# Optimization experiments

Hardware: AMD Instinct MI355X
Metric: run time of the kernel (lower is better)

## Reference

```python
import jax, jax.numpy as jnp
import numpy as np

N_QUBITS = 10
INPUT_DIM = 49
ENC_LAMBDA = float(np.pi)
ENC_BETA_MAX = 1.0
BATCH = 2048
LOGIT_SCALE_MIN, LOGIT_SCALE_MAX = 0.5, 80.0
LOGIT_CLAMP = 30.0

# arch_mat rows: [control, target, op, axis, feature]; op: ENC=1, ROT=2, CNOT=3; 1-indexed, 0=none.
def _build_arch_mat():
    cols = []
    for b in range(3):
        for q in range(N_QUBITS):  # encoding RY gates
            cols.append((0, q + 1, 1, 2, (b * N_QUBITS + q) % INPUT_DIM + 1))
        for q in range(N_QUBITS):  # trainable RX gates
            cols.append((0, q + 1, 2, 1, 0))
        for q in range(N_QUBITS - 1):  # CNOT chain
            cols.append((q + 1, q + 2, 3, 0, 0))
    return np.asarray(cols, dtype=np.int64).T  # (5, L)

ARCH_MAT = _build_arch_mat()
N_THETA = int(((ARCH_MAT[2] == 2) & (ARCH_MAT[1] > 0) & (ARCH_MAT[3] > 0)).sum())


def _apply_rot(state, ax, q, theta):
    # state: (B, 2,...,2) complex64; theta: scalar or (B,)
    st = jnp.moveaxis(state, 1 + q, -1)
    half = 0.5 * theta
    c, s = jnp.cos(half), jnp.sin(half)
    if c.ndim == 1:  # per-sample angle -> broadcast over remaining qubit axes
        shape = (-1,) + (1,) * (st.ndim - 2)
        c, s = c.reshape(shape), s.reshape(shape)
    s0, s1 = st[..., 0], st[..., 1]
    if ax == 1:  # RX
        n0 = c * s0 - 1j * s * s1
        n1 = c * s1 - 1j * s * s0
    elif ax == 2:  # RY
        n0 = c * s0 - s * s1
        n1 = c * s1 + s * s0
    else:  # RZ
        n0 = (c - 1j * s) * s0
        n1 = (c + 1j * s) * s1
    return jnp.moveaxis(jnp.stack([n0, n1], axis=-1), -1, 1 + q)


def _apply_cnot(state, cq, tq):
    st = jnp.moveaxis(state, (1 + cq, 1 + tq), (-2, -1))
    st = jnp.stack([st[..., 0, :], st[..., 1, ::-1]], axis=-2)
    return jnp.moveaxis(st, (-2, -1), (1 + cq, 1 + tq))


def _circuit(x, theta, enc_alpha_raw, enc_beta_raw):
    B = x.shape[0]
    state = jnp.zeros((B,) + (2,) * N_QUBITS, jnp.complex64)
    state = state.at[(slice(None),) + (0,) * N_QUBITS].set(1.0)
    alpha = jax.nn.softplus(enc_alpha_raw) + 1e-6  # (D,)
    beta = jnp.tanh(enc_beta_raw) * ENC_BETA_MAX   # (D,)
    rot_idx = 0
    for l in range(ARCH_MAT.shape[1]):  # static structural loop over gates
        c, t, op, ax, f1 = (int(v) for v in ARCH_MAT[:, l])
        if op == 1 and t > 0 and ax > 0 and f1 > 0:
            fi = f1 - 1
            ang = ENC_LAMBDA * (alpha[fi] * x[:, fi] + beta[fi])  # (B,)
            state = _apply_rot(state, ax, t - 1, ang)
        elif op == 2 and t > 0 and ax > 0:
            state = _apply_rot(state, ax, t - 1, theta[rot_idx])
            rot_idx += 1
        elif op == 3 and c > 0 and t > 0 and c != t:
            state = _apply_cnot(state, c - 1, t - 1)
    probs = state.real ** 2 + state.imag ** 2  # (B, 2,...,2)
    exps = []
    for q in range(N_QUBITS):  # <Z_q> = p(q=0) - p(q=1)
        p = jnp.moveaxis(probs, 1 + q, -1).reshape(B, -1, 2).sum(axis=1)
        exps.append(p[:, 0] - p[:, 1])
    return jnp.stack(exps, axis=1)  # (B, n_qubits)


def setup_inputs() -> dict:
    key = jax.random.key(0)
    k = jax.random.split(key, 4)
    x = jax.random.normal(k[0], (BATCH, INPUT_DIM), jnp.float32)
    theta = jnp.clip(0.01 * jax.random.normal(k[1], (N_THETA,), jnp.float32), -0.1, 0.1)
    a0 = float(np.log(np.exp(1.0) - 1.0))  # softplus^-1(enc_alpha_init=1.0)
    enc_alpha_raw = jnp.full((INPUT_DIM,), a0, jnp.float32)
    enc_beta_raw = jnp.zeros((INPUT_DIM,), jnp.float32)  # arctanh(0)=0
    head_w = 0.02 * jax.random.normal(k[2], (1, N_QUBITS), jnp.float32)
    bound = 1.0 / float(np.sqrt(N_QUBITS))
    head_b = jax.random.uniform(k[3], (1,), jnp.float32, -bound, bound)
    logit_scale = jnp.asarray(1.0, jnp.float32)
    return {"x": x, "theta": theta, "enc_alpha_raw": enc_alpha_raw, "enc_beta_raw": enc_beta_raw,
            "head_w": head_w, "head_b": head_b, "logit_scale": logit_scale}


def reference(x, theta, enc_alpha_raw, enc_beta_raw, head_w, head_b, logit_scale):
    exps = _circuit(x, theta, enc_alpha_raw, enc_beta_raw)  # (B, n_qubits)
    raw = exps @ head_w.T + head_b                          # (B, 1)
    scale = jnp.clip(logit_scale, LOGIT_SCALE_MIN, LOGIT_SCALE_MAX)
    return jnp.clip(scale * raw, -LOGIT_CLAMP, LOGIT_CLAMP)
```

## Files before the change

### kernel.cpp

```cpp
#include <hip/hip_runtime.h>
#include <math.h>


#define PI_F 3.14159265358979323846f

typedef unsigned v2u __attribute__((ext_vector_type(2)));

#if defined(__has_builtin)
#if __has_builtin(__builtin_amdgcn_permlane16_swap)
#define HAVE_PL16 1
#endif
#if __has_builtin(__builtin_amdgcn_permlane32_swap)
#define HAVE_PL32 1
#endif
#endif

__device__ __forceinline__ float rdlane(float v, int l) {
    return __int_as_float(__builtin_amdgcn_readlane(__float_as_int(v), l));
}

__device__ __forceinline__ float xor1p(float v) {
    return __int_as_float(__builtin_amdgcn_update_dpp(
        0, __float_as_int(v), 0xB1, 0xF, 0xF, true));
}
__device__ __forceinline__ float xor2p(float v) {
    return __int_as_float(__builtin_amdgcn_update_dpp(
        0, __float_as_int(v), 0x4E, 0xF, 0xF, true));
}
__device__ __forceinline__ float xor4p(float v) {
    int t = __builtin_amdgcn_update_dpp(0, __float_as_int(v), 0x1B, 0xF, 0xF, true);
    t = __builtin_amdgcn_update_dpp(0, t, 0x141, 0xF, 0xF, true);
    return __int_as_float(t);
}
__device__ __forceinline__ float xor8p(float v) {
    return __int_as_float(__builtin_amdgcn_update_dpp(
        0, __float_as_int(v), 0x128, 0xF, 0xF, true));
}
__device__ __forceinline__ float xor16p(float v, bool hi) {
#ifdef HAVE_PL16
    v2u r = __builtin_amdgcn_permlane16_swap(
        (unsigned)__float_as_int(v), (unsigned)__float_as_int(v), false, false);
    return __int_as_float((int)(hi ? r.x : r.y));
#else
    return __shfl_xor(v, 16);
#endif
}
__device__ __forceinline__ float xor32p(float v, bool hi) {
#ifdef HAVE_PL32
    v2u r = __builtin_amdgcn_permlane32_swap(
        (unsigned)__float_as_int(v), (unsigned)__float_as_int(v), false, false);
    return __int_as_float((int)(hi ? r.x : r.y));
#else
    return __shfl_xor(v, 32);
#endif
}

template<int Q>
__device__ __forceinline__ float lane_xor(float v, bool hi) {
    if constexpr (Q == 0) return xor1p(v);
    else if constexpr (Q == 1) return xor2p(v);
    else if constexpr (Q == 2) return xor4p(v);
    else if constexpr (Q == 3) return xor8p(v);
    else if constexpr (Q == 4) return xor16p(v, hi);
    else return xor32p(v, hi);
}

template<bool NEG>
__device__ __forceinline__ float2 cgate(const float2 ar2, const float2 ai2,
                                        const float2 br2, const float2 bi2,
                                        const float2 v, const float2 w) {
    float2 acc;
    asm("v_pk_mul_f32 %0, %1, %2" : "=v"(acc) : "v"(ar2), "v"(v));
    if constexpr (!NEG) {
        asm("v_pk_fma_f32 %0, %1, %2, %0 op_sel:[0,1,0] op_sel_hi:[1,0,1] neg_lo:[0,1,0]"
            : "+v"(acc) : "v"(ai2), "v"(v));
        asm("v_pk_fma_f32 %0, %1, %2, %0" : "+v"(acc) : "v"(br2), "v"(w));
    } else {
        asm("v_pk_fma_f32 %0, %1, %2, %0 op_sel:[0,1,0] op_sel_hi:[1,0,1] neg_lo:[1,1,0] neg_hi:[1,0,0]"
            : "+v"(acc) : "v"(ai2), "v"(v));
        asm("v_pk_fma_f32 %0, %1, %2, %0 neg_lo:[1,0,0] neg_hi:[1,0,0]"
            : "+v"(acc) : "v"(br2), "v"(w));
    }
    asm("v_pk_fma_f32 %0, %1, %2, %0 op_sel:[0,1,0] op_sel_hi:[1,0,1] neg_lo:[0,1,0]"
        : "+v"(acc) : "v"(bi2), "v"(w));
    return acc;
}

template<int Q>
__device__ __forceinline__ void lane_gate(float2 (&st)[8], int lane,
                                          float ar, float ai, float br, float bi) {
    const bool hi = (lane & (1 << Q)) != 0;
    const float aiL = hi ? -ai : ai;
    const float brL = hi ? -br : br;
    const float2 ar2 = make_float2(ar, ar);
    const float2 ai2 = make_float2(aiL, aiL);
    const float2 br2 = make_float2(brL, brL);
    const float2 bi2 = make_float2(bi, bi);
    #pragma unroll
    for (int r = 0; r < 8; ++r) {
        float2 p;
        p.x = lane_xor<Q>(st[r].x, hi);
        p.y = lane_xor<Q>(st[r].y, hi);
        st[r] = cgate<false>(ar2, ai2, br2, bi2, st[r], p);
    }
}

template<int RB>
__device__ __forceinline__ void reg_gate(float2 (&st)[8],
                                         float ar, float ai, float br, float bi) {
    const float2 ar2 = make_float2(ar, ar);
    const float2 ai2 = make_float2(ai, ai);
    const float2 br2 = make_float2(br, br);
    const float2 bi2 = make_float2(bi, bi);
    #pragma unroll
    for (int r = 0; r < 8; ++r) {
        if ((r & RB) == 0) {
            const int r1 = r | RB;
            const float2 v0 = st[r], v1 = st[r1];
            st[r]  = cgate<false>(ar2, ai2, br2, bi2, v0, v1);
            st[r1] = cgate<true >(ar2, ai2, br2, bi2, v1, v0);
        }
    }
}

__global__ __launch_bounds__(256, 4) void cqv_kernel(
    const float* __restrict__ x,
    const float* __restrict__ theta,
    const float* __restrict__ alpha_raw,
    const float* __restrict__ beta_raw,
    const float* __restrict__ head_w,
    const float* __restrict__ head_b,
    const float* __restrict__ logit_scale,
    float* __restrict__ out,
    int batch)
{
    const int lane = threadIdx.x & 63;
    const int wavid = threadIdx.x >> 6;
    const int p  = wavid >> 1;
    const int wv = wavid & 1;
    const int s = blockIdx.x * 2 + p;
    if (s >= batch) return;

    __shared__ float2 lds[2][2][8][2][64];
    __shared__ float pbuf[2][2];

    const int l5 = (lane >> 5) & 1;
    const int srcLane = lane ^ ((lane & 31) << 1);

    const int g = (lane < 30) ? lane : 0;
    const float alpha = log1pf(__expf(alpha_raw[g])) + 1e-6f;
    const float beta  = tanhf(beta_raw[g]);
    const float halfE = 0.5f * PI_F * (alpha * x[s * 49 + g] + beta);
    float cE, sE, cT, sT;
    __sincosf(halfE, &sE, &cE);
    __sincosf(0.5f * theta[g], &sT, &cT);

    float2 st[8];

    {
        float u0r[10], u0i[10], u1r[10], u1i[10];
        #pragma unroll
        for (int q = 0; q < 10; ++q) {
            const float ce = rdlane(cE, q), se = rdlane(sE, q);
            const float ct = rdlane(cT, q), s_t = rdlane(sT, q);
            u0r[q] = ct * ce;  u0i[q] = -s_t * se;
            u1r[q] = ct * se;  u1i[q] = -s_t * ce;
        }
        float plr = 1.f, pli = 0.f;
        #pragma unroll
        for (int q = 0; q < 6; ++q) {
            const bool bq = (lane >> q) & 1;
            const float wr = bq ? u1r[q] : u0r[q];
            const float wi = bq ? u1i[q] : u0i[q];
            const float nr = plr * wr - pli * wi;
            const float ni = plr * wi + pli * wr;
            plr = nr; pli = ni;
        }
        const float w9r = wv ? u1r[9] : u0r[9], w9i = wv ? u1i[9] : u0i[9];
        float t67r[4], t67i[4], t89r[2], t89i[2];
        #pragma unroll
        for (int a = 0; a < 4; ++a) {
            const float w6r = (a & 1) ? u1r[6] : u0r[6], w6i = (a & 1) ? u1i[6] : u0i[6];
            const float w7r = (a & 2) ? u1r[7] : u0r[7], w7i = (a & 2) ? u1i[7] : u0i[7];
            t67r[a] = w6r * w7r - w6i * w7i;  t67i[a] = w6r * w7i + w6i * w7r;
        }
        #pragma unroll
        for (int k = 0; k < 2; ++k) {
            const float w8r = k ? u1r[8] : u0r[8], w8i = k ? u1i[8] : u0i[8];
            t89r[k] = w8r * w9r - w8i * w9i;  t89i[k] = w8r * w9i + w8i * w9r;
        }
        #pragma unroll
        for (int r = 0; r < 8; ++r) {
            const float ar = t67r[r & 3] * t89r[r >> 2] - t67i[r & 3] * t89i[r >> 2];
            const float ai = t67r[r & 3] * t89i[r >> 2] + t67i[r & 3] * t89r[r >> 2];
            st[r].x = ar * plr - ai * pli;
            st[r].y = ar * pli + ai * plr;
        }
    }

    {
        #pragma unroll
        for (int r = 0; r < 8; ++r) lds[0][p][r][wv][lane] = st[r];
        __syncthreads();
        #pragma unroll
        for (int r = 0; r < 8; ++r) {
            const int sReg = (r ^ ((r & 3) << 1)) ^ l5;
            const int k9 = wv ^ (r >> 2);
            st[r] = lds[0][p][sReg][k9][srcLane];
        }
    }

    #pragma unroll 1
    for (int b = 1; b < 3; ++b) {
        const int base = b * 10;
#define GATE_PARAMS(Q) \
        const float ce = rdlane(cE, base + (Q)), se = rdlane(sE, base + (Q)); \
        const float ct = rdlane(cT, base + (Q)), s_t = rdlane(sT, base + (Q));
#define APPLY_LANE_GATE(Q) { GATE_PARAMS(Q) \
        lane_gate<Q>(st, lane, ct * ce, -s_t * se, -ct * se, -s_t * ce); }
#define APPLY_REG_GATE(Q, RB) { GATE_PARAMS(Q) \
        reg_gate<RB>(st, ct * ce, -s_t * se, -ct * se, -s_t * ce); }
        APPLY_LANE_GATE(0)
        APPLY_LANE_GATE(1)
        APPLY_LANE_GATE(2)
        APPLY_LANE_GATE(3)
        APPLY_LANE_GATE(4)
        APPLY_LANE_GATE(5)
        APPLY_REG_GATE(6, 1)
        APPLY_REG_GATE(7, 2)
        APPLY_REG_GATE(8, 4)

        const int db = b & 1;
        GATE_PARAMS(9)
        const float ar = ct * ce, ai = -s_t * se, br = -ct * se, bi = -s_t * ce;
        const float2 ar2 = make_float2(ar, ar), ai2 = make_float2(ai, ai);
        const float2 br2 = make_float2(br, br), bi2 = make_float2(bi, bi);
        #pragma unroll
        for (int r = 0; r < 8; ++r) lds[db][p][r][wv][lane] = st[r];
        __syncthreads();
        #pragma unroll
        for (int r = 0; r < 8; ++r) {
            const int sReg = (r ^ ((r & 3) << 1)) ^ l5;
            const int k9 = wv ^ (r >> 2);
            const float2 v = lds[db][p][sReg][k9][srcLane];
            const float2 w = lds[db][p][sReg][k9 ^ 1][srcLane];
            if (k9 == 0) st[r] = cgate<false>(ar2, ai2, br2, bi2, v, w);
            else         st[r] = cgate<true >(ar2, ai2, br2, bi2, v, w);
        }
#undef GATE_PARAMS
#undef APPLY_LANE_GATE
#undef APPLY_REG_GATE
    }

    float w[10];
    #pragma unroll
    for (int q = 0; q < 10; ++q) w[q] = head_w[q];
    float wlane = wv ? -w[9] : w[9];
    #pragma unroll
    for (int q = 0; q < 6; ++q) wlane += ((lane >> q) & 1) ? -w[q] : w[q];
    float acc = 0.f, psum = 0.f;
    #pragma unroll
    for (int r = 0; r < 8; ++r) {
        const float pw = st[r].x * st[r].x + st[r].y * st[r].y;
        const float wr = ((r & 1) ? -w[6] : w[6]) + ((r & 2) ? -w[7] : w[7])
                       + ((r & 4) ? -w[8] : w[8]);
        psum += pw;
        acc = fmaf(wr, pw, acc);
    }
    float partial = fmaf(wlane, psum, acc);
    #pragma unroll
    for (int off = 32; off >= 1; off >>= 1) partial += __shfl_xor(partial, off);

    if (lane == 0) pbuf[p][wv] = partial;
    __syncthreads();
    if (lane == 0 && wv == 0) {
        const float scale = fminf(fmaxf(logit_scale[0], 0.5f), 80.f);
        const float raw = pbuf[p][0] + pbuf[p][1] + head_b[0];
        out[s] = fminf(fmaxf(scale * raw, -30.f), 30.f);
    }
}

extern "C" void kernel_launch(void* const* d_in, const int* in_sizes, int n_in,
                              void* d_out, int out_size, void* d_ws, size_t ws_size,
                              hipStream_t stream) {
    const int B = in_sizes[0] / 49;
    dim3 block(256);
    dim3 grid((B + 1) / 2);
    cqv_kernel<<<grid, block, 0, stream>>>(
        (const float*)d_in[0], (const float*)d_in[1], (const float*)d_in[2],
        (const float*)d_in[3], (const float*)d_in[4], (const float*)d_in[5],
        (const float*)d_in[6], (float*)d_out, B);
}
```

Baseline: 81.23 us.

## Use one sample per block and skip the final qubit-transpose via parity-aware readout

Launches one 128-thread block per sample instead of packing two samples into a 256-thread block, so each __syncthreads only spans two waves. The last layer's LDS exchange now reads only the partner wave's value at the same index rather than permuting lanes and registers. The Z-expectation readout is rewritten with prefix-parity signs so it works in the untransposed layout. This trims shuffle and address work in the final stage but doubles the block count and carries a risk of sign errors in the parity mapping.

```diff
diff --git a/kernel.cpp b/kernel.cpp
--- a/kernel.cpp
+++ b/kernel.cpp
@@ -123,7 +123,7 @@
     }
 }
 
-__global__ __launch_bounds__(256, 4) void cqv_kernel(
+__global__ __launch_bounds__(128, 4) void cqv_kernel(
     const float* __restrict__ x,
     const float* __restrict__ theta,
     const float* __restrict__ alpha_raw,
@@ -135,14 +135,11 @@
     int batch)
 {
     const int lane = threadIdx.x & 63;
-    const int wavid = threadIdx.x >> 6;
-    const int p  = wavid >> 1;
-    const int wv = wavid & 1;
-    const int s = blockIdx.x * 2 + p;
-    if (s >= batch) return;
-
-    __shared__ float2 lds[2][2][8][2][64];
-    __shared__ float pbuf[2][2];
+    const int wv = threadIdx.x >> 6;
+    const int s = blockIdx.x;
+
+    __shared__ float2 lds[2][8][2][64];
+    __shared__ float pbuf[2];
 
     const int l5 = (lane >> 5) & 1;
     const int srcLane = lane ^ ((lane & 31) << 1);
@@ -200,82 +197,101 @@
 
     {
         #pragma unroll
-        for (int r = 0; r < 8; ++r) lds[0][p][r][wv][lane] = st[r];
+        for (int r = 0; r < 8; ++r) lds[0][r][wv][lane] = st[r];
         __syncthreads();
         #pragma unroll
         for (int r = 0; r < 8; ++r) {
             const int sReg = (r ^ ((r & 3) << 1)) ^ l5;
             const int k9 = wv ^ (r >> 2);
-            st[r] = lds[0][p][sReg][k9][srcLane];
-        }
-    }
-
-    #pragma unroll 1
-    for (int b = 1; b < 3; ++b) {
-        const int base = b * 10;
-#define GATE_PARAMS(Q) \
-        const float ce = rdlane(cE, base + (Q)), se = rdlane(sE, base + (Q)); \
-        const float ct = rdlane(cT, base + (Q)), s_t = rdlane(sT, base + (Q));
-#define APPLY_LANE_GATE(Q) { GATE_PARAMS(Q) \
+            st[r] = lds[0][sReg][k9][srcLane];
+        }
+    }
+
+#define GATE_PARAMS(BASE, Q) \
+        const float ce = rdlane(cE, (BASE) + (Q)), se = rdlane(sE, (BASE) + (Q)); \
+        const float ct = rdlane(cT, (BASE) + (Q)), s_t = rdlane(sT, (BASE) + (Q));
+#define APPLY_LANE_GATE(BASE, Q) { GATE_PARAMS(BASE, Q) \
         lane_gate<Q>(st, lane, ct * ce, -s_t * se, -ct * se, -s_t * ce); }
-#define APPLY_REG_GATE(Q, RB) { GATE_PARAMS(Q) \
+#define APPLY_REG_GATE(BASE, Q, RB) { GATE_PARAMS(BASE, Q) \
         reg_gate<RB>(st, ct * ce, -s_t * se, -ct * se, -s_t * ce); }
-        APPLY_LANE_GATE(0)
-        APPLY_LANE_GATE(1)
-        APPLY_LANE_GATE(2)
-        APPLY_LANE_GATE(3)
-        APPLY_LANE_GATE(4)
-        APPLY_LANE_GATE(5)
-        APPLY_REG_GATE(6, 1)
-        APPLY_REG_GATE(7, 2)
-        APPLY_REG_GATE(8, 4)
-
-        const int db = b & 1;
-        GATE_PARAMS(9)
+#define APPLY_Q0_Q8(BASE) \
+        APPLY_LANE_GATE(BASE, 0) APPLY_LANE_GATE(BASE, 1) APPLY_LANE_GATE(BASE, 2) \
+        APPLY_LANE_GATE(BASE, 3) APPLY_LANE_GATE(BASE, 4) APPLY_LANE_GATE(BASE, 5) \
+        APPLY_REG_GATE(BASE, 6, 1) APPLY_REG_GATE(BASE, 7, 2) APPLY_REG_GATE(BASE, 8, 4)
+
+    {
+        APPLY_Q0_Q8(10)
+        GATE_PARAMS(10, 9)
         const float ar = ct * ce, ai = -s_t * se, br = -ct * se, bi = -s_t * ce;
         const float2 ar2 = make_float2(ar, ar), ai2 = make_float2(ai, ai);
         const float2 br2 = make_float2(br, br), bi2 = make_float2(bi, bi);
         #pragma unroll
-        for (int r = 0; r < 8; ++r) lds[db][p][r][wv][lane] = st[r];
+        for (int r = 0; r < 8; ++r) lds[1][r][wv][lane] = st[r];
         __syncthreads();
         #pragma unroll
         for (int r = 0; r < 8; ++r) {
             const int sReg = (r ^ ((r & 3) << 1)) ^ l5;
             const int k9 = wv ^ (r >> 2);
-            const float2 v = lds[db][p][sReg][k9][srcLane];
-            const float2 w = lds[db][p][sReg][k9 ^ 1][srcLane];
+            const float2 v = lds[1][sReg][k9][srcLane];
+            const float2 w = lds[1][sReg][k9 ^ 1][srcLane];
             if (k9 == 0) st[r] = cgate<false>(ar2, ai2, br2, bi2, v, w);
             else         st[r] = cgate<true >(ar2, ai2, br2, bi2, v, w);
         }
+    }
+
+    {
+        APPLY_Q0_Q8(20)
+        GATE_PARAMS(20, 9)
+        const float ar = ct * ce, ai = -s_t * se, br = -ct * se, bi = -s_t * ce;
+        const float2 ar2 = make_float2(ar, ar), ai2 = make_float2(ai, ai);
+        const float2 br2 = make_float2(br, br), bi2 = make_float2(bi, bi);
+        #pragma unroll
+        for (int r = 0; r < 8; ++r) lds[0][r][wv][lane] = st[r];
+        __syncthreads();
+        #pragma unroll
+        for (int r = 0; r < 8; ++r) {
+            const float2 w = lds[0][r][wv ^ 1][lane];
+            if (wv == 0) st[r] = cgate<false>(ar2, ai2, br2, bi2, st[r], w);
+            else         st[r] = cgate<true >(ar2, ai2, br2, bi2, st[r], w);
+        }
+    }
 #undef GATE_PARAMS
 #undef APPLY_LANE_GATE
 #undef APPLY_REG_GATE
-    }
+#undef APPLY_Q0_Q8
 
     float w[10];
     #pragma unroll
     for (int q = 0; q < 10; ++q) w[q] = head_w[q];
-    float wlane = wv ? -w[9] : w[9];
-    #pragma unroll
-    for (int q = 0; q < 6; ++q) wlane += ((lane >> q) & 1) ? -w[q] : w[q];
+    float wlane = 0.f;
+    {
+        int pref = 0;
+        #pragma unroll
+        for (int q = 0; q < 6; ++q) {
+            pref ^= (lane >> q) & 1;
+            wlane += pref ? -w[q] : w[q];
+        }
+    }
+    const float sPL = ((__builtin_popcount(lane & 63) & 1) ? -1.f : 1.f);
     float acc = 0.f, psum = 0.f;
     #pragma unroll
     for (int r = 0; r < 8; ++r) {
         const float pw = st[r].x * st[r].x + st[r].y * st[r].y;
-        const float wr = ((r & 1) ? -w[6] : w[6]) + ((r & 2) ? -w[7] : w[7])
-                       + ((r & 4) ? -w[8] : w[8]);
+        const int p0 = r & 1, p1 = p0 ^ ((r >> 1) & 1), p2 = p1 ^ ((r >> 2) & 1);
+        const float wr = (p0 ? -w[6] : w[6]) + (p1 ? -w[7] : w[7])
+                       + (p2 ? -w[8] : w[8]) + ((p2 ^ wv) ? -w[9] : w[9]);
         psum += pw;
         acc = fmaf(wr, pw, acc);
     }
-    float partial = fmaf(wlane, psum, acc);
+    float partial = fmaf(wlane, psum, sPL * acc);
     #pragma unroll
     for (int off = 32; off >= 1; off >>= 1) partial += __shfl_xor(partial, off);
 
-    if (lane == 0) pbuf[p][wv] = partial;
+    if (lane == 0) pbuf[wv] = partial;
     __syncthreads();
-    if (lane == 0 && wv == 0) {
+    if (threadIdx.x == 0) {
         const float scale = fminf(fmaxf(logit_scale[0], 0.5f), 80.f);
-        const float raw = pbuf[p][0] + pbuf[p][1] + head_b[0];
+        const float raw = pbuf[0] + pbuf[1] + head_b[0];
         out[s] = fminf(fmaxf(scale * raw, -30.f), 30.f);
     }
 }
@@ -284,8 +300,8 @@
                               void* d_out, int out_size, void* d_ws, size_t ws_size,
                               hipStream_t stream) {
     const int B = in_sizes[0] / 49;
-    dim3 block(256);
-    dim3 grid((B + 1) / 2);
+    dim3 block(128);
+    dim3 grid(B);
     cqv_kernel<<<grid, block, 0, stream>>>(
         (const float*)d_in[0], (const float*)d_in[1], (const float*)d_in[2],
         (const float*)d_in[3], (const float*)d_in[4], (const float*)d_in[5],
```

Result: no change. 79.74 us (-1.8%).
